# Performance work log

Hardware: AMD Instinct MI355X
Metric: run time of the kernel (lower is better)

The kernel has to match this reference:

```python
import jax, jax.numpy as jnp
import numpy as np

NEG_SLOPE = 0.2
EPS = 1e-16


def _add_self_loops(edge_index, num_nodes):
    loop = jnp.arange(num_nodes, dtype=edge_index.dtype)
    return jnp.concatenate([edge_index, jnp.stack([loop, loop])], axis=1)


def gat_conv(x, edge_index, W, a_src, a_dst, b, concat):
    """PyG-style GATConv: gather -> attention logits -> segment softmax -> scatter-add."""
    N = x.shape[0]
    H, C = a_src.shape
    xl = (x @ W).reshape(N, H, C)                       # [N,H,C]
    alpha_src = (xl * a_src[None]).sum(-1)              # [N,H]
    alpha_dst = (xl * a_dst[None]).sum(-1)              # [N,H]
    src, dst = edge_index[0], edge_index[1]
    alpha = jax.nn.leaky_relu(alpha_src[src] + alpha_dst[dst], NEG_SLOPE)  # [E,H]
    amax = jax.ops.segment_max(alpha, dst, num_segments=N)
    amax = jnp.where(jnp.isfinite(amax), amax, 0.0)
    ea = jnp.exp(alpha - amax[dst])
    denom = jax.ops.segment_sum(ea, dst, num_segments=N)
    attn = ea / (denom[dst] + EPS)                      # [E,H]
    msg = xl[src] * attn[:, :, None]                    # [E,H,C]
    out = jax.ops.segment_sum(msg, dst, num_segments=N)  # [N,H,C]
    out = out.reshape(N, H * C) if concat else out.mean(axis=1)
    return out + b


def setup_inputs() -> dict:
    key = jax.random.key(0)
    ks = jax.random.split(key, 9)
    N, F, E, H, C, NC = 100000, 128, 1600000, 8, 8, 40
    s = lambda fan: 1.0 / np.sqrt(fan)
    return {
        "x": jax.random.normal(ks[0], (N, F), dtype=jnp.float32),
        "edge_index": jax.random.randint(ks[1], (2, E), 0, N, dtype=jnp.int64),
        "W1": jax.random.normal(ks[2], (F, H * C), dtype=jnp.float32) * s(F),
        "a_src1": jax.random.normal(ks[3], (H, C), dtype=jnp.float32) * s(C),
        "a_dst1": jax.random.normal(ks[4], (H, C), dtype=jnp.float32) * s(C),
        "b1": jnp.zeros((H * C,), dtype=jnp.float32),
        "W2": jax.random.normal(ks[5], (H * C, NC), dtype=jnp.float32) * s(H * C),
        "a_src2": jax.random.normal(ks[6], (1, NC), dtype=jnp.float32) * s(NC),
        "a_dst2": jax.random.normal(ks[7], (1, NC), dtype=jnp.float32) * s(NC),
        "b2": jnp.zeros((NC,), dtype=jnp.float32),
    }


def reference(x, edge_index, W1, a_src1, a_dst1, b1, W2, a_src2, a_dst2, b2):
    N = x.shape[0]
    ei = _add_self_loops(edge_index, N)
    h = gat_conv(x, ei, W1, a_src1, a_dst1, b1, concat=True)   # [N,64]
    h = jax.nn.elu(h)
    out = gat_conv(h, ei, W2, a_src2, a_dst2, b2, concat=True)  # [N,nclass]
    return out
```

## Files before the change

kernel.cpp:

```cpp
#include <hip/hip_runtime.h>
#include <math.h>

#define NEG_SLOPE 0.2f
#define GAT_EPS 1e-16f
#define LOG2E 1.44269504088896340736f

#define CH   8192
#define NBK  256

__device__ __forceinline__ unsigned pack_bf16(float a, float b) {
    unsigned ua = __float_as_uint(a);
    unsigned ub = __float_as_uint(b);
    ua = (ua + 0x8000u) >> 16;
    ub = (ub + 0x8000u) & 0xffff0000u;
    return ua | ub;
}
__device__ __forceinline__ float bf_lo(unsigned pk) {
    return __uint_as_float(pk << 16);
}
__device__ __forceinline__ float bf_hi(unsigned pk) {
    return __uint_as_float(pk & 0xffff0000u);
}


__global__ __launch_bounds__(256) void k_place(
    const int* __restrict__ ei, int E, int N, int shift,
    const int* __restrict__ cnt, int NCHv,
    unsigned* __restrict__ bslab)
{
    __shared__ int cur[NBK];
    __shared__ int cs[NBK];
    int c = blockIdx.x;
    int t = threadIdx.x;
    int pre = 0, tot = 0;
    for (int cc = 0; cc < NCHv; cc++) {
        int v = cnt[cc * NBK + t];
        tot += v;
        if (cc < c) pre += v;
    }
    cs[t] = tot;
    __syncthreads();
    for (int o = 1; o < 256; o <<= 1) {
        int v = (t >= o) ? cs[t - o] : 0;
        __syncthreads();
        cs[t] += v;
        __syncthreads();
    }
    cur[t] = (cs[t] - tot) + pre;
    __syncthreads();

    int Etot = E + N;
    int base = c * CH;
    int lim = min(base + CH, Etot);
    int mask = (1 << shift) - 1;
    for (int e = base + threadIdx.x; e < lim; e += 256) {
        int s, d;
        if (e < E) { s = ei[e]; d = ei[E + e]; }
        else       { s = e - E; d = s; }
        int b = d >> shift;
        int pos = atomicAdd(&cur[b], 1);
        bslab[pos] = (unsigned)s | ((unsigned)(d & mask) << 17);
    }
}

__global__ __launch_bounds__(256) void k_csr2(
    const int* __restrict__ cnt, int NCHv,
    const unsigned* __restrict__ bslab,
    int shift, int* __restrict__ row_ptr, int* __restrict__ csr_src,
    int N, int Etot)
{
    __shared__ int sdeg[1024];
    __shared__ int scur[1024];
    __shared__ int ps[256];
    __shared__ int bbs[NBK + 1];
    int b = blockIdx.x;
    int tid = threadIdx.x;

    int tot = 0;
    for (int cc = 0; cc < NCHv; cc++) tot += cnt[cc * NBK + tid];
    ps[tid] = tot;
    __syncthreads();
    for (int o = 1; o < 256; o <<= 1) {
        int v = (tid >= o) ? ps[tid - o] : 0;
        __syncthreads();
        ps[tid] += v;
        __syncthreads();
    }
    bbs[tid] = ps[tid] - tot;
    if (tid == 255) bbs[256] = ps[255];
    __syncthreads();

    int beg = bbs[b], end = bbs[b + 1];
    int nodes = 1 << shift;
    int node0 = b << shift;
    for (int i = tid; i < nodes; i += 256) sdeg[i] = 0;
    __syncthreads();
    for (int i = beg + tid; i < end; i += 256)
        atomicAdd(&sdeg[bslab[i] >> 17], 1);
    __syncthreads();
    int per = (nodes + 255) / 256;
    int mybase = tid * per;
    int sum = 0;
    for (int j = 0; j < per; j++) sum += sdeg[mybase + j];
    ps[tid] = sum;
    __syncthreads();
    int v0 = ps[tid];
    for (int o = 1; o < 256; o <<= 1) {
        int v = (tid >= o) ? ps[tid - o] : 0;
        __syncthreads();
        ps[tid] += v;
        __syncthreads();
    }
    int run = ps[tid] - v0;
    for (int j = 0; j < per; j++) {
        int i = mybase + j;
        int dgi = sdeg[i];
        scur[i] = beg + run;
        int node = node0 + i;
        if (node < N) row_ptr[node] = beg + run;
        run += dgi;
    }
    if (b == 0 && tid == 0) row_ptr[N] = Etot;
    __syncthreads();
    for (int i = beg + tid; i < end; i += 256) {
        unsigned w = bslab[i];
        int pos = atomicAdd(&scur[w >> 17], 1);
        csr_src[pos] = (int)(w & 0x1FFFFu);
    }
}

__global__ __launch_bounds__(256) void k_gemm1(
    const float* __restrict__ x, const float* __restrict__ W1,
    const float* __restrict__ a_src1, const float* __restrict__ a_dst1,
    unsigned* __restrict__ xl1b, float* __restrict__ as1,
    float* __restrict__ ad1, int N, int F,
    const int* __restrict__ ei, int E, int shift, int NCHv,
    int* __restrict__ cnt)
{
    __shared__ float Ws[128 * 64];
    __shared__ float asrc[64];
    __shared__ float adst[64];
    __shared__ int hist[NBK];

    if (blockIdx.x < NCHv) {
        hist[threadIdx.x] = 0;
        __syncthreads();
        int Etot = E + N;
        int base = blockIdx.x * CH;
        int lim = min(base + CH, Etot);
        for (int e = base + threadIdx.x; e < lim; e += 256) {
            int d = (e < E) ? ei[E + e] : (e - E);
            atomicAdd(&hist[d >> shift], 1);
        }
        __syncthreads();
        cnt[blockIdx.x * NBK + threadIdx.x] = hist[threadIdx.x];
    }

    for (int i = threadIdx.x; i < F * 64; i += 256) Ws[i] = W1[i];
    if (threadIdx.x < 64) {
        asrc[threadIdx.x] = a_src1[threadIdx.x];
        adst[threadIdx.x] = a_dst1[threadIdx.x];
    }
    __syncthreads();

    int n = blockIdx.x * 64 + (threadIdx.x >> 2);
    int q = threadIdx.x & 3;
    if (n >= N) return;
    int c0 = q * 16;

    float acc[16];
#pragma unroll
    for (int c = 0; c < 16; c++) acc[c] = 0.0f;

    const float4* xr4 = (const float4*)(x + (size_t)n * F);
    for (int k4 = 0; k4 < F / 4; k4++) {
        float4 xv = xr4[k4];
        const float* w0 = &Ws[(k4 * 4 + 0) * 64 + c0];
        const float* w1 = &Ws[(k4 * 4 + 1) * 64 + c0];
        const float* w2 = &Ws[(k4 * 4 + 2) * 64 + c0];
        const float* w3 = &Ws[(k4 * 4 + 3) * 64 + c0];
#pragma unroll
        for (int c = 0; c < 16; c++) {
            float a = acc[c];
            a = fmaf(xv.x, w0[c], a);
            a = fmaf(xv.y, w1[c], a);
            a = fmaf(xv.z, w2[c], a);
            a = fmaf(xv.w, w3[c], a);
            acc[c] = a;
        }
    }

    uint4 pk0, pk1;
    pk0.x = pack_bf16(acc[0], acc[1]);  pk0.y = pack_bf16(acc[2], acc[3]);
    pk0.z = pack_bf16(acc[4], acc[5]);  pk0.w = pack_bf16(acc[6], acc[7]);
    pk1.x = pack_bf16(acc[8], acc[9]);  pk1.y = pack_bf16(acc[10], acc[11]);
    pk1.z = pack_bf16(acc[12], acc[13]); pk1.w = pack_bf16(acc[14], acc[15]);
    uint4* xo = (uint4*)(xl1b + (size_t)n * 32 + q * 8);
    xo[0] = pk0;
    xo[1] = pk1;

#pragma unroll
    for (int hh = 0; hh < 2; hh++) {
        float s = 0.0f, t = 0.0f;
#pragma unroll
        for (int c = 0; c < 8; c++) {
            s = fmaf(acc[hh * 8 + c], asrc[c0 + hh * 8 + c], s);
            t = fmaf(acc[hh * 8 + c], adst[c0 + hh * 8 + c], t);
        }
        as1[(size_t)n * 8 + 2 * q + hh] = s * LOG2E;
        ad1[(size_t)n * 8 + 2 * q + hh] = t * LOG2E;
    }
}

__global__ __launch_bounds__(256) void k_agg1(
    const int* __restrict__ row_ptr, const int* __restrict__ csr_src,
    const float* __restrict__ as1, const float* __restrict__ ad1,
    const unsigned* __restrict__ xl1b, const float* __restrict__ b1,
    float* __restrict__ h1, int N)
{
    int d = blockIdx.x * 8 + ((threadIdx.x >> 6) << 1) + ((threadIdx.x >> 5) & 1);
    if (d >= N) return;
    int lane = threadIdx.x & 31;
    int g = lane >> 3;
    int l = lane & 7;

    int beg = row_ptr[d], end = row_ptr[d + 1];
    float adh = ad1[(size_t)d * 8 + l];

    float ax[8];
#pragma unroll
    for (int j = 0; j < 8; j++) ax[j] = 0.f;
    float den = 0.f;

    int i = beg + g;
    for (; i + 4 < end; i += 8) {
        int s0 = csr_src[i];
        int s1 = csr_src[i + 4];
        size_t q0 = (size_t)s0 * 8 + l;
        size_t q1 = (size_t)s1 * 8 + l;
        float al0 = as1[q0] + adh;
        float al1 = as1[q1] + adh;
        uint4 k0 = *(const uint4*)(xl1b + (q0 << 2));
        uint4 k1 = *(const uint4*)(xl1b + (q1 << 2));
        al0 = fmaxf(al0, NEG_SLOPE * al0);
        al1 = fmaxf(al1, NEG_SLOPE * al1);
        float e0 = __builtin_amdgcn_exp2f(al0);
        float e1 = __builtin_amdgcn_exp2f(al1);
        ax[0] = fmaf(e0, bf_lo(k0.x), ax[0]);
        ax[1] = fmaf(e0, bf_hi(k0.x), ax[1]);
        ax[2] = fmaf(e0, bf_lo(k0.y), ax[2]);
        ax[3] = fmaf(e0, bf_hi(k0.y), ax[3]);
        ax[4] = fmaf(e0, bf_lo(k0.z), ax[4]);
        ax[5] = fmaf(e0, bf_hi(k0.z), ax[5]);
        ax[6] = fmaf(e0, bf_lo(k0.w), ax[6]);
        ax[7] = fmaf(e0, bf_hi(k0.w), ax[7]);
        ax[0] = fmaf(e1, bf_lo(k1.x), ax[0]);
        ax[1] = fmaf(e1, bf_hi(k1.x), ax[1]);
        ax[2] = fmaf(e1, bf_lo(k1.y), ax[2]);
        ax[3] = fmaf(e1, bf_hi(k1.y), ax[3]);
        ax[4] = fmaf(e1, bf_lo(k1.z), ax[4]);
        ax[5] = fmaf(e1, bf_hi(k1.z), ax[5]);
        ax[6] = fmaf(e1, bf_lo(k1.w), ax[6]);
        ax[7] = fmaf(e1, bf_hi(k1.w), ax[7]);
        den += e0 + e1;
    }
    if (i < end) {
        int s0 = csr_src[i];
        size_t q0 = (size_t)s0 * 8 + l;
        float al0 = as1[q0] + adh;
        uint4 k0 = *(const uint4*)(xl1b + (q0 << 2));
        al0 = fmaxf(al0, NEG_SLOPE * al0);
        float e0 = __builtin_amdgcn_exp2f(al0);
        ax[0] = fmaf(e0, bf_lo(k0.x), ax[0]);
        ax[1] = fmaf(e0, bf_hi(k0.x), ax[1]);
        ax[2] = fmaf(e0, bf_lo(k0.y), ax[2]);
        ax[3] = fmaf(e0, bf_hi(k0.y), ax[3]);
        ax[4] = fmaf(e0, bf_lo(k0.z), ax[4]);
        ax[5] = fmaf(e0, bf_hi(k0.z), ax[5]);
        ax[6] = fmaf(e0, bf_lo(k0.w), ax[6]);
        ax[7] = fmaf(e0, bf_hi(k0.w), ax[7]);
        den += e0;
    }

#pragma unroll
    for (int m = 8; m < 32; m <<= 1) {
#pragma unroll
        for (int j = 0; j < 8; j++) ax[j] += __shfl_xor(ax[j], m);
        den += __shfl_xor(den, m);
    }

    if (g == 0) {
        float inv = __builtin_amdgcn_rcpf(den + GAT_EPS);
        const float4* bb = (const float4*)(b1 + l * 8);
        float4 b0 = bb[0], b1v = bb[1];
        float4 o0, o1;
        float v;
        v = fmaf(ax[0], inv, b0.x);  o0.x = v > 0.f ? v : __expf(v) - 1.f;
        v = fmaf(ax[1], inv, b0.y);  o0.y = v > 0.f ? v : __expf(v) - 1.f;
        v = fmaf(ax[2], inv, b0.z);  o0.z = v > 0.f ? v : __expf(v) - 1.f;
        v = fmaf(ax[3], inv, b0.w);  o0.w = v > 0.f ? v : __expf(v) - 1.f;
        v = fmaf(ax[4], inv, b1v.x); o1.x = v > 0.f ? v : __expf(v) - 1.f;
        v = fmaf(ax[5], inv, b1v.y); o1.y = v > 0.f ? v : __expf(v) - 1.f;
        v = fmaf(ax[6], inv, b1v.z); o1.z = v > 0.f ? v : __expf(v) - 1.f;
        v = fmaf(ax[7], inv, b1v.w); o1.w = v > 0.f ? v : __expf(v) - 1.f;
        float4* op = (float4*)(h1 + (size_t)d * 64 + l * 8);
        op[0] = o0;
        op[1] = o1;
    }
}

__global__ __launch_bounds__(256) void k_node2(
    const float* __restrict__ h1, const float* __restrict__ W2,
    const float* __restrict__ a_src2, const float* __restrict__ a_dst2,
    unsigned* __restrict__ xl2b, float* __restrict__ ad2, int N)
{
    __shared__ float Ws[64 * 40];
    __shared__ float a2s[40];
    __shared__ float a2d[40];
    for (int i = threadIdx.x; i < 64 * 40; i += 256) Ws[i] = W2[i];
    if (threadIdx.x < 40) {
        a2s[threadIdx.x] = a_src2[threadIdx.x];
        a2d[threadIdx.x] = a_dst2[threadIdx.x];
    }
    __syncthreads();

    int n = blockIdx.x * 128 + (threadIdx.x >> 1);
    int q = threadIdx.x & 1;
    if (n >= N) return;
    int c0 = q * 20;

    float o[20];
#pragma unroll
    for (int j = 0; j < 20; j++) o[j] = 0.0f;

    const float4* hr4 = (const float4*)(h1 + (size_t)n * 64);
    for (int k4 = 0; k4 < 16; k4++) {
        float4 hv = hr4[k4];
        const float* w0 = &Ws[(k4 * 4 + 0) * 40 + c0];
        const float* w1 = &Ws[(k4 * 4 + 1) * 40 + c0];
        const float* w2 = &Ws[(k4 * 4 + 2) * 40 + c0];
        const float* w3 = &Ws[(k4 * 4 + 3) * 40 + c0];
#pragma unroll
        for (int j = 0; j < 20; j++) {
            float a = o[j];
            a = fmaf(hv.x, w0[j], a);
            a = fmaf(hv.y, w1[j], a);
            a = fmaf(hv.z, w2[j], a);
            a = fmaf(hv.w, w3[j], a);
            o[j] = a;
        }
    }

    float s = 0.0f, t = 0.0f;
#pragma unroll
    for (int j = 0; j < 20; j++) {
        s = fmaf(o[j], a2s[c0 + j], s);
        t = fmaf(o[j], a2d[c0 + j], t);
    }
    s += __shfl_xor(s, 1);
    t += __shfl_xor(t, 1);
    if (q == 0) {
        xl2b[(size_t)n * 24 + 20] = __float_as_uint(s * LOG2E);
        ad2[n] = t * LOG2E;
    }

    unsigned* xo = xl2b + (size_t)n * 24 + q * 10;
#pragma unroll
    for (int p = 0; p < 10; p++) xo[p] = pack_bf16(o[2 * p], o[2 * p + 1]);
}

__global__ __launch_bounds__(256) void k_agg2(
    const int* __restrict__ row_ptr, const int* __restrict__ csr_src,
    const float* __restrict__ ad2,
    const unsigned* __restrict__ xl2b, const float* __restrict__ b2,
    float* __restrict__ out, int N)
{
    int d = blockIdx.x * 8 + ((threadIdx.x >> 6) << 1) + ((threadIdx.x >> 5) & 1);
    if (d >= N) return;
    int lane = threadIdx.x & 31;
    int g = lane >> 3;
    int l = lane & 7;
    if (l >= 5) return;

    int beg = row_ptr[d], end = row_ptr[d + 1];
    float add = ad2[d];

    float ax[8];
#pragma unroll
    for (int j = 0; j < 8; j++) ax[j] = 0.f;
    float den = 0.f;

    int i = beg + g;
    for (; i + 4 < end; i += 8) {
        int s0 = csr_src[i];
        int s1 = csr_src[i + 4];
        const unsigned* r0 = xl2b + (size_t)s0 * 24;
        const unsigned* r1 = xl2b + (size_t)s1 * 24;
        float al0 = __uint_as_float(r0[20]) + add;
        float al1 = __uint_as_float(r1[20]) + add;
        uint4 k0 = *(const uint4*)(r0 + l * 4);
        uint4 k1 = *(const uint4*)(r1 + l * 4);
        al0 = fmaxf(al0, NEG_SLOPE * al0);
        al1 = fmaxf(al1, NEG_SLOPE * al1);
        float e0 = __builtin_amdgcn_exp2f(al0);
        float e1 = __builtin_amdgcn_exp2f(al1);
        ax[0] = fmaf(e0, bf_lo(k0.x), ax[0]);
        ax[1] = fmaf(e0, bf_hi(k0.x), ax[1]);
        ax[2] = fmaf(e0, bf_lo(k0.y), ax[2]);
        ax[3] = fmaf(e0, bf_hi(k0.y), ax[3]);
        ax[4] = fmaf(e0, bf_lo(k0.z), ax[4]);
        ax[5] = fmaf(e0, bf_hi(k0.z), ax[5]);
        ax[6] = fmaf(e0, bf_lo(k0.w), ax[6]);
        ax[7] = fmaf(e0, bf_hi(k0.w), ax[7]);
        ax[0] = fmaf(e1, bf_lo(k1.x), ax[0]);
        ax[1] = fmaf(e1, bf_hi(k1.x), ax[1]);
        ax[2] = fmaf(e1, bf_lo(k1.y), ax[2]);
        ax[3] = fmaf(e1, bf_hi(k1.y), ax[3]);
        ax[4] = fmaf(e1, bf_lo(k1.z), ax[4]);
        ax[5] = fmaf(e1, bf_hi(k1.z), ax[5]);
        ax[6] = fmaf(e1, bf_lo(k1.w), ax[6]);
        ax[7] = fmaf(e1, bf_hi(k1.w), ax[7]);
        den += e0 + e1;
    }
    if (i < end) {
        int s0 = csr_src[i];
        const unsigned* r0 = xl2b + (size_t)s0 * 24;
        float al0 = __uint_as_float(r0[20]) + add;
        uint4 k0 = *(const uint4*)(r0 + l * 4);
        al0 = fmaxf(al0, NEG_SLOPE * al0);
        float e0 = __builtin_amdgcn_exp2f(al0);
        ax[0] = fmaf(e0, bf_lo(k0.x), ax[0]);
        ax[1] = fmaf(e0, bf_hi(k0.x), ax[1]);
        ax[2] = fmaf(e0, bf_lo(k0.y), ax[2]);
        ax[3] = fmaf(e0, bf_hi(k0.y), ax[3]);
        ax[4] = fmaf(e0, bf_lo(k0.z), ax[4]);
        ax[5] = fmaf(e0, bf_hi(k0.z), ax[5]);
        ax[6] = fmaf(e0, bf_lo(k0.w), ax[6]);
        ax[7] = fmaf(e0, bf_hi(k0.w), ax[7]);
        den += e0;
    }

#pragma unroll
    for (int m = 8; m < 32; m <<= 1) {
#pragma unroll
        for (int j = 0; j < 8; j++) ax[j] += __shfl_xor(ax[j], m);
        den += __shfl_xor(den, m);
    }

    if (g == 0) {
        float inv = __builtin_amdgcn_rcpf(den + GAT_EPS);
        float* op = out + (size_t)d * 40 + l * 8;
        const float* bb = b2 + l * 8;
#pragma unroll
        for (int j = 0; j < 8; j++) op[j] = fmaf(ax[j], inv, bb[j]);
    }
}

extern "C" void kernel_launch(void* const* d_in, const int* in_sizes, int n_in,
                              void* d_out, int out_size, void* d_ws, size_t ws_size,
                              hipStream_t stream) {
    const float* x      = (const float*)d_in[0];
    const int*   ei     = (const int*)d_in[1];
    const float* W1     = (const float*)d_in[2];
    const float* a_src1 = (const float*)d_in[3];
    const float* a_dst1 = (const float*)d_in[4];
    const float* b1     = (const float*)d_in[5];
    const float* W2     = (const float*)d_in[6];
    const float* a_src2 = (const float*)d_in[7];
    const float* a_dst2 = (const float*)d_in[8];
    const float* b2     = (const float*)d_in[9];

    int F = in_sizes[2] / 64;
    int N = in_sizes[0] / F;
    int E = in_sizes[1] / 2;
    int Etot = E + N;
    int NCHv = (Etot + CH - 1) / CH;
    int shift = 9;
    while (((N - 1) >> shift) >= NBK) shift++;

    unsigned* xl1b    = (unsigned*)d_ws;
    float*    h1      = (float*)(xl1b + (size_t)N * 32);
    float*    as1     = h1 + (size_t)N * 64;
    float*    ad1     = as1 + (size_t)N * 8;
    int*      row_ptr = (int*)(ad1 + (size_t)N * 8);
    int*      csr_src = row_ptr + (N + 1);
    int*      cnt     = csr_src + Etot;
    unsigned* bslab   = (unsigned*)(cnt + (size_t)NCHv * NBK);
    unsigned* xl2b    = xl1b;
    float*    ad2     = ad1;

    int gridG1 = (N + 63) / 64;
    if (gridG1 < NCHv) gridG1 = NCHv;
    k_gemm1<<<gridG1, 256, 0, stream>>>(x, W1, a_src1, a_dst1,
                                        xl1b, as1, ad1, N, F,
                                        ei, E, shift, NCHv, cnt);

    k_place<<<NCHv, 256, 0, stream>>>(ei, E, N, shift, cnt, NCHv, bslab);
    k_csr2 <<<NBK, 256, 0, stream>>>(cnt, NCHv, bslab, shift,
                                     row_ptr, csr_src, N, Etot);

    k_agg1 <<<(N + 7) / 8, 256, 0, stream>>>(row_ptr, csr_src, as1, ad1,
                                             xl1b, b1, h1, N);

    k_node2<<<(N + 127) / 128, 256, 0, stream>>>(h1, W2, a_src2, a_dst2,
                                                 xl2b, ad2, N);
    k_agg2 <<<(N + 7) / 8, 256, 0, stream>>>(row_ptr, csr_src, ad2,
                                             xl2b, b2, (float*)d_out, N);
}
```

Baseline: 335.2 us.

## Add separate offset-scan kernel and use smaller chunks with more buckets in CSR build

Adds a kernel that computes per-bucket exclusive offsets across chunks once, instead of every k_place and k_csr2 block rescanning the whole count matrix serially. Chunk size drops and bucket count doubles, giving more placement blocks and smaller per-bucket node ranges. The count and offset arrays now live in the h1 buffer, which is reused before h1 is written. This costs one extra kernel launch and a larger count matrix in exchange for removing the redundant O(chunks) serial loops.

Result: faster. 300.8 us (-10.3%).

```diff
diff --git a/kernel.cpp b/kernel.cpp
--- a/kernel.cpp
+++ b/kernel.cpp
@@ -5,8 +5,8 @@
 #define GAT_EPS 1e-16f
 #define LOG2E 1.44269504088896340736f
 
-#define CH   8192
-#define NBK  256
+#define CH   2048
+#define NBK  512
 
 __device__ __forceinline__ unsigned pack_bf16(float a, float b) {
     unsigned ua = __float_as_uint(a);
@@ -23,37 +23,63 @@
 }
 
 
+__global__ __launch_bounds__(256) void k_off_a(
+    const int* __restrict__ cnt, int* __restrict__ off,
+    int* __restrict__ tot, int NCHv)
+{
+    __shared__ int sm[256];
+    int b = blockIdx.x;
+    int t = threadIdx.x;
+    int carry = 0;
+    for (int c0 = 0; c0 < NCHv; c0 += 256) {
+        int c = c0 + t;
+        int v = (c < NCHv) ? cnt[c * NBK + b] : 0;
+        sm[t] = v;
+        __syncthreads();
+        for (int o = 1; o < 256; o <<= 1) {
+            int add = (t >= o) ? sm[t - o] : 0;
+            __syncthreads();
+            sm[t] += add;
+            __syncthreads();
+        }
+        if (c < NCHv) off[c * NBK + b] = carry + sm[t] - v;
+        carry += sm[255];
+        __syncthreads();
+    }
+    if (t == 0) tot[b] = carry;
+}
+
 __global__ __launch_bounds__(256) void k_place(
     const int* __restrict__ ei, int E, int N, int shift,
-    const int* __restrict__ cnt, int NCHv,
+    const int* __restrict__ off, const int* __restrict__ tot,
     unsigned* __restrict__ bslab)
 {
     __shared__ int cur[NBK];
-    __shared__ int cs[NBK];
+    __shared__ int ps[256];
     int c = blockIdx.x;
     int t = threadIdx.x;
-    int pre = 0, tot = 0;
-    for (int cc = 0; cc < NCHv; cc++) {
-        int v = cnt[cc * NBK + t];
-        tot += v;
-        if (cc < c) pre += v;
-    }
-    cs[t] = tot;
-    __syncthreads();
-    for (int o = 1; o < 256; o <<= 1) {
-        int v = (t >= o) ? cs[t - o] : 0;
-        __syncthreads();
-        cs[t] += v;
-        __syncthreads();
-    }
-    cur[t] = (cs[t] - tot) + pre;
+    int carry = 0;
+    for (int b0 = 0; b0 < NBK; b0 += 256) {
+        int v = tot[b0 + t];
+        ps[t] = v;
+        __syncthreads();
+        for (int o = 1; o < 256; o <<= 1) {
+            int u = (t >= o) ? ps[t - o] : 0;
+            __syncthreads();
+            ps[t] += u;
+            __syncthreads();
+        }
+        cur[b0 + t] = carry + ps[t] - v + off[(size_t)c * NBK + b0 + t];
+        carry += ps[255];
+        __syncthreads();
+    }
     __syncthreads();
 
     int Etot = E + N;
     int base = c * CH;
     int lim = min(base + CH, Etot);
     int mask = (1 << shift) - 1;
-    for (int e = base + threadIdx.x; e < lim; e += 256) {
+    for (int e = base + t; e < lim; e += 256) {
         int s, d;
         if (e < E) { s = ei[e]; d = ei[E + e]; }
         else       { s = e - E; d = s; }
@@ -64,33 +90,36 @@
 }
 
 __global__ __launch_bounds__(256) void k_csr2(
-    const int* __restrict__ cnt, int NCHv,
-    const unsigned* __restrict__ bslab,
+    const int* __restrict__ tot, const unsigned* __restrict__ bslab,
     int shift, int* __restrict__ row_ptr, int* __restrict__ csr_src,
     int N, int Etot)
 {
     __shared__ int sdeg[1024];
     __shared__ int scur[1024];
     __shared__ int ps[256];
-    __shared__ int bbs[NBK + 1];
+    __shared__ int bb[NBK + 1];
     int b = blockIdx.x;
     int tid = threadIdx.x;
 
-    int tot = 0;
-    for (int cc = 0; cc < NCHv; cc++) tot += cnt[cc * NBK + tid];
-    ps[tid] = tot;
-    __syncthreads();
-    for (int o = 1; o < 256; o <<= 1) {
-        int v = (tid >= o) ? ps[tid - o] : 0;
-        __syncthreads();
-        ps[tid] += v;
-        __syncthreads();
-    }
-    bbs[tid] = ps[tid] - tot;
-    if (tid == 255) bbs[256] = ps[255];
-    __syncthreads();
-
-    int beg = bbs[b], end = bbs[b + 1];
+    int carry = 0;
+    for (int b0 = 0; b0 < NBK; b0 += 256) {
+        int v = tot[b0 + tid];
+        ps[tid] = v;
+        __syncthreads();
+        for (int o = 1; o < 256; o <<= 1) {
+            int u = (tid >= o) ? ps[tid - o] : 0;
+            __syncthreads();
+            ps[tid] += u;
+            __syncthreads();
+        }
+        bb[b0 + tid] = carry + ps[tid] - v;
+        carry += ps[255];
+        __syncthreads();
+    }
+    if (tid == 0) bb[NBK] = carry;
+    __syncthreads();
+
+    int beg = bb[b], end = bb[b + 1];
     int nodes = 1 << shift;
     int node0 = b << shift;
     for (int i = tid; i < nodes; i += 256) sdeg[i] = 0;
@@ -143,7 +172,7 @@
     __shared__ int hist[NBK];
 
     if (blockIdx.x < NCHv) {
-        hist[threadIdx.x] = 0;
+        for (int i = threadIdx.x; i < NBK; i += 256) hist[i] = 0;
         __syncthreads();
         int Etot = E + N;
         int base = blockIdx.x * CH;
@@ -153,7 +182,8 @@
             atomicAdd(&hist[d >> shift], 1);
         }
         __syncthreads();
-        cnt[blockIdx.x * NBK + threadIdx.x] = hist[threadIdx.x];
+        for (int i = threadIdx.x; i < NBK; i += 256)
+            cnt[(size_t)blockIdx.x * NBK + i] = hist[i];
     }
 
     for (int i = threadIdx.x; i < F * 64; i += 256) Ws[i] = W1[i];
@@ -475,7 +505,7 @@
     int E = in_sizes[1] / 2;
     int Etot = E + N;
     int NCHv = (Etot + CH - 1) / CH;
-    int shift = 9;
+    int shift = 8;
     while (((N - 1) >> shift) >= NBK) shift++;
 
     unsigned* xl1b    = (unsigned*)d_ws;
@@ -484,8 +514,10 @@
     float*    ad1     = as1 + (size_t)N * 8;
     int*      row_ptr = (int*)(ad1 + (size_t)N * 8);
     int*      csr_src = row_ptr + (N + 1);
-    int*      cnt     = csr_src + Etot;
-    unsigned* bslab   = (unsigned*)(cnt + (size_t)NCHv * NBK);
+    unsigned* bslab   = (unsigned*)(csr_src + Etot);
+    int*      cnt     = (int*)h1;
+    int*      off     = cnt + (size_t)NCHv * NBK;
+    int*      tot     = off + (size_t)NCHv * NBK;
     unsigned* xl2b    = xl1b;
     float*    ad2     = ad1;
 
@@ -495,8 +527,9 @@
                                         xl1b, as1, ad1, N, F,
                                         ei, E, shift, NCHv, cnt);
 
-    k_place<<<NCHv, 256, 0, stream>>>(ei, E, N, shift, cnt, NCHv, bslab);
-    k_csr2 <<<NBK, 256, 0, stream>>>(cnt, NCHv, bslab, shift,
+    k_off_a<<<NBK, 256, 0, stream>>>(cnt, off, tot, NCHv);
+    k_place<<<NCHv, 256, 0, stream>>>(ei, E, N, shift, off, tot, bslab);
+    k_csr2 <<<NBK, 256, 0, stream>>>(tot, bslab, shift,
                                      row_ptr, csr_src, N, Etot);
 
     k_agg1 <<<(N + 7) / 8, 256, 0, stream>>>(row_ptr, csr_src, as1, ad1,
```
